# Optimization experiments

Measured on AMD Instinct MI355X. Metric: run time of the kernel, lower is better.

The kernel has to match this reference:

```python
import jax, jax.numpy as jnp
import numpy as np
from jax.scipy.linalg import solve_triangular

N, K, D = 131072, 8, 32  # samples, clusters, dims


def setup_inputs() -> dict:
    key = jax.random.key(0)
    k1, k2, k3, k4 = jax.random.split(key, 4)
    return {
        "X": jax.random.normal(k1, (N, D), dtype=jnp.float32),
        "mu": jax.random.normal(k2, (K, D), dtype=jnp.float32),
        "L": jax.random.normal(k3, (K, D, D), dtype=jnp.float32),
        "weights": jax.random.normal(k4, (K,), dtype=jnp.float32),
        "it": 0,
    }


def _mixture_log_likelihoods(X, mu, L, weights):
    K_, D_ = mu.shape
    LOG2PI = float(np.log(2.0 * np.pi))
    # update_covariances: A_k = L_k L_k^T + I  (always SPD -> cholesky succeeds)
    A = jnp.einsum('kab,kcb->kac', L, L) + jnp.eye(D_, dtype=L.dtype)
    Lc = jnp.linalg.cholesky(A)            # [K,D,D] lower Cholesky factors
    invLc = jnp.linalg.inv(Lc)             # [K,D,D]
    # all cluster pairs (cartesian_prod order: i outer, j inner)
    ii, jj = [g.reshape(-1) for g in jnp.meshgrid(jnp.arange(K_), jnp.arange(K_), indexing='ij')]
    Si, Sj = Lc[ii], Lc[jj]                # NOTE: original uses the CHOLESKY FACTORS here
    invSi, invSj = invLc[ii], invLc[jj]
    mui, muj = mu[ii], mu[jj]
    # _gaussian_product: sigma = inv(inv(Si)+inv(Sj)); mu = sigma @ (inv(Si) mu_i + inv(Sj) mu_j)
    sigma = jnp.linalg.inv(invSi + invSj)                      # [P,D,D]
    rhs = jnp.einsum('pab,pb->pa', invSi, mui) + jnp.einsum('pab,pb->pa', invSj, muj)
    mu_p = jnp.einsum('pab,pb->pa', sigma, rhs)                # [P,D]
    # _product_z: log(1/sqrt(det(2*pi*(Si+Sj))) * exp(-0.5 dmu^T inv(Si+Sj) dmu))
    S = Si + Sj
    dmu = mui - muj
    quad = -0.5 * jnp.einsum('pa,pab,pb->p', dmu, jnp.linalg.inv(S), dmu)
    z = -0.5 * jnp.log(jnp.linalg.det(2.0 * np.pi * S)) + quad  # [P]
    # _unormalised_pdf: lower-triangular solve against sigma (only lower triangle used)
    diff = X[None, :, :] - mu_p[:, None, :]                    # [P,N,D]
    m = solve_triangular(sigma, jnp.swapaxes(diff, 1, 2), lower=True)  # [P,D,N]
    ll = -0.5 * (jnp.sum(m * m, axis=1) + D_ * LOG2PI
                 + jnp.log(jnp.linalg.det(sigma))[:, None])    # [P,N]
    logw = jax.nn.log_softmax(weights)                         # softmax weights, then log
    logprob = z[:, None] + ll + logw[ii][:, None] + logw[jj][:, None]  # [P,N]
    return jnp.log(jnp.sum(jnp.exp(logprob), axis=0))          # [N]


def reference(X, mu, L, weights, it):
    ll = _mixture_log_likelihoods(X, mu, L, weights)
    return jax.scipy.special.logsumexp(ll, axis=0)  # scalar
```

## Files before the change

### kernel.cpp

```cpp
#include <hip/hip_runtime.h>

#define D 32
#define K 8
#define NPAIR 36
#define PROWS 576

#define PMOFF 0
#define WOFF 4608
#define C2OFF 4864
#define CMAXOFF 4900
#define LCOFF 4928
#define PARTOFF 13120

typedef float v2f __attribute__((ext_vector_type(2)));

__host__ __device__ constexpr int gidx(int i, int j) {
    return i * 8 + j - i * (i + 1) / 2;
}
__host__ __device__ constexpr int proff(int r) {
    return 4 * (r / 4 + 1) * (2 * (r / 4) + (r % 4));
}

__global__ __launch_bounds__(64) void setup1_kernel(
    const float* __restrict__ mu, const float* __restrict__ L,
    float* __restrict__ ws)
{
    __shared__ float sA[D][D + 1];
    __shared__ float sLc[D][D + 1];
    __shared__ float sI[D][D + 1];
    const int k = blockIdx.x;
    const int tid = threadIdx.x;
    const int i = tid & 31;

    for (int e = tid; e < D * D; e += 64) sI[e >> 5][e & 31] = L[k * D * D + e];
    __syncthreads();

    for (int e = tid; e < D * D; e += 64) {
        const int a = e >> 5, c = e & 31;
        float s = (a == c) ? 1.0f : 0.0f;
        #pragma unroll
        for (int b = 0; b < D; ++b) s = fmaf(sI[a][b], sI[c][b], s);
        sA[a][c] = s;
    }
    __syncthreads();

    float lrow[D];
    #pragma unroll
    for (int j = 0; j < D; ++j) {
        if (i == j) {
            float s = sA[j][j];
            #pragma unroll
            for (int b = 0; b < j; ++b) s = fmaf(-lrow[b], lrow[b], s);
            const float d = sqrtf(s);
            lrow[j] = d;
            #pragma unroll
            for (int b = 0; b < j; ++b) sLc[j][b] = lrow[b];
            sLc[j][j] = d;
        }
        __syncthreads();
        if (i > j) {
            float s = sA[i][j];
            #pragma unroll
            for (int b = 0; b < j; ++b) s = fmaf(-lrow[b], sLc[j][b], s);
            lrow[j] = s / sLc[j][j];
        }
    }
    __syncthreads();

    for (int e = tid; e < D * D; e += 64) {
        const int r = e >> 5, c = e & 31;
        ws[LCOFF + k * D * D + e] = (c <= r) ? sLc[r][c] : 0.0f;
    }

    {
        const int j = i;
        #pragma unroll
        for (int ii = 0; ii < D; ++ii) {
            float s = (ii == j) ? 1.0f : 0.0f;
            #pragma unroll
            for (int b = 0; b < ii; ++b) s = fmaf(-sLc[ii][b], sI[b][j], s);
            const float cii = s / sLc[ii][ii];
            sI[ii][j] = cii;
            const int w4 = 4 * (ii / 4 + 1);
            if (j < w4) ws[PMOFF + k * PROWS + proff(ii) + j] = cii;
        }
    }
    __syncthreads();

    {
        float s = 0.0f;
        #pragma unroll
        for (int b = 0; b < D; ++b) s = fmaf(sI[i][b], mu[k * D + b], s);
        ws[WOFF + k * D + i] = s;
    }
}

#define SLC(kk, r, c) sLc2[(kk) * 1024 + (r) * 32 + (c)]

__global__ __launch_bounds__(256) void setup2_kernel(
    const float* __restrict__ mu, const float* __restrict__ weights,
    float* __restrict__ ws)
{
    __shared__ float sLc2[K * D * D];
    __shared__ float sMu[K * D];
    __shared__ float sWt[K];
    __shared__ float sLogw[K];
    __shared__ float sCp[NPAIR];
    __shared__ float sCmax;
    const int tid = threadIdx.x;

    {
        const float4* src = (const float4*)(ws + LCOFF);
        float4* dst = (float4*)sLc2;
        #pragma unroll
        for (int e = 0; e < 8; ++e) dst[tid + 256 * e] = src[tid + 256 * e];
        sMu[tid] = mu[tid];
        if (tid < K) sWt[tid] = weights[tid];
    }
    __syncthreads();

    if (tid == 0) {
        float m = -INFINITY;
        for (int t = 0; t < K; ++t) m = fmaxf(m, sWt[t]);
        float s = 0.0f;
        for (int t = 0; t < K; ++t) s += expf(sWt[t] - m);
        const float lse = m + logf(s);
        for (int t = 0; t < K; ++t) sLogw[t] = sWt[t] - lse;
    }
    __syncthreads();

    if (tid < NPAIR) {
        int tt = tid, pi = 0;
        while (tt >= (K - pi)) { tt -= (K - pi); ++pi; }
        const int pj = pi + tt;
        const float LOG2PI = 1.8378770664093453f;
        float sumlogS = 0.0f, logdetsig = 0.0f;
        #pragma unroll
        for (int r = 0; r < D; ++r) {
            const float di = SLC(pi, r, r), dj = SLC(pj, r, r);
            sumlogS += logf(di + dj);
            logdetsig -= logf(1.0f / di + 1.0f / dj);
        }
        float v[D];
        float quad_acc = 0.0f;
        #pragma unroll
        for (int r = 0; r < D; ++r) {
            const float d0 = sMu[pi * D + r] - sMu[pj * D + r];
            float s = d0;
            #pragma unroll
            for (int b = 0; b < r; ++b)
                s = fmaf(-(SLC(pi, r, b) + SLC(pj, r, b)), v[b], s);
            v[r] = s / (SLC(pi, r, r) + SLC(pj, r, r));
            quad_acc = fmaf(d0, v[r], quad_acc);
        }
        const float quad = -0.5f * quad_acc;
        float c = quad - 0.5f * sumlogS - (float)D * LOG2PI - 0.5f * logdetsig
                  + sLogw[pi] + sLogw[pj];
        if (pi < pj) c += 0.6931471805599453f;
        sCp[tid] = c;
    }
    __syncthreads();
    if (tid == 0) {
        float m = -INFINITY;
        for (int t = 0; t < NPAIR; ++t) m = fmaxf(m, sCp[t]);
        sCmax = m;
        ws[CMAXOFF] = m;
    }
    __syncthreads();
    if (tid < NPAIR)
        ws[C2OFF + tid] = (sCp[tid] - sCmax) * 1.4426950408889634f;
}

#define XCHG 4864

__global__ __launch_bounds__(128, 2) void main_kernel(
    const float* __restrict__ X, const float* __restrict__ cst,
    float* __restrict__ partials, int nsamp)
{
    __shared__ __align__(16) float sBig[XCHG];
    __shared__ __align__(16) float sW[K * D];
    __shared__ float sC2[NPAIR];
    const int tid = threadIdx.x;
    const int wv = tid >> 6;
    const int lane = tid & 63;

    const int n0 = blockIdx.x * 128 + lane;
    const int n1 = n0 + 64;
    const int m0 = (n0 < nsamp) ? n0 : 0;
    const int m1 = (n1 < nsamp) ? n1 : 0;

    v2f xa[16], xb[16];
    {
        const float4* Xv0 = (const float4*)(X + m0 * D);
        const float4* Xv1 = (const float4*)(X + m1 * D);
        #pragma unroll
        for (int q = 0; q < 8; ++q) {
            const float4 t0 = Xv0[q];
            xa[2 * q]     = (v2f){t0.x, t0.y};
            xa[2 * q + 1] = (v2f){t0.z, t0.w};
            const float4 t1 = Xv1[q];
            xb[2 * q]     = (v2f){t1.x, t1.y};
            xb[2 * q + 1] = (v2f){t1.z, t1.w};
        }
    }

    {
        const float4* src = (const float4*)cst;
        float4* dst = (float4*)sBig;
        for (int e = tid; e < K * PROWS / 4; e += 128) dst[e] = src[e];
        const float4* srcw = (const float4*)(cst + WOFF);
        float4* dstw = (float4*)sW;
        if (tid < K * D / 4) dstw[tid] = srcw[tid];
        if (tid < NPAIR) sC2[tid] = cst[C2OFF + tid];
    }
    __syncthreads();

    v2f G2[NPAIR];
    #pragma unroll
    for (int t = 0; t < NPAIR; ++t) G2[t] = (v2f){0.0f, 0.0f};

    #pragma unroll
    for (int rh = 0; rh < 8; ++rh) {
        if ((rh & 1) == wv) {
            #pragma unroll
            for (int rr = 0; rr < 4; ++rr) {
                const int r = 4 * rh + rr;
                v2f ya[K], yb[K];
                #pragma unroll
                for (int k = 0; k < K; ++k) {
                    const float wvv = sW[k * D + r];
                    v2f a0 = (v2f){-wvv, 0.0f};
                    v2f a1 = (v2f){-wvv, 0.0f};
                    const float* Mr = sBig + k * PROWS + proff(r);
                    #pragma unroll
                    for (int c4 = 0; c4 <= rh; ++c4) {
                        const float4 m4 = *(const float4*)(Mr + 4 * c4);
                        const v2f mlo = (v2f){m4.x, m4.y};
                        const v2f mhi = (v2f){m4.z, m4.w};
                        a0 = __builtin_elementwise_fma(mlo, xa[2 * c4],     a0);
                        a1 = __builtin_elementwise_fma(mlo, xb[2 * c4],     a1);
                        a0 = __builtin_elementwise_fma(mhi, xa[2 * c4 + 1], a0);
                        a1 = __builtin_elementwise_fma(mhi, xb[2 * c4 + 1], a1);
                    }
                    ya[k] = a0;  yb[k] = a1;
                }
                v2f y2[K];
                #pragma unroll
                for (int k = 0; k < K; ++k)
                    y2[k] = (v2f){ya[k].x + ya[k].y, yb[k].x + yb[k].y};
                #pragma unroll
                for (int pi = 0; pi < K; ++pi)
                    #pragma unroll
                    for (int pj = pi; pj < K; ++pj)
                        G2[gidx(pi, pj)] = __builtin_elementwise_fma(
                            y2[pi], y2[pj], G2[gidx(pi, pj)]);
            }
        }
    }

    __syncthreads();

    if (wv == 1) {
        float2* xch = (float2*)sBig;
        #pragma unroll
        for (int t = 0; t < NPAIR; ++t)
            xch[t * 65 + lane] = make_float2(G2[t].x, G2[t].y);
    }
    __syncthreads();

    if (wv == 0) {
        const float2* xch = (const float2*)sBig;
        #pragma unroll
        for (int t = 0; t < NPAIR; ++t) {
            const float2 g = xch[t * 65 + lane];
            G2[t] += (v2f){g.x, g.y};
        }

        v2f acc2 = (v2f){0.0f, 0.0f};
        const float NH = -0.72134752044448170f;
        #pragma unroll
        for (int pi = 0; pi < K; ++pi)
            #pragma unroll
            for (int pj = pi; pj < K; ++pj) {
                const v2f q2 = __builtin_elementwise_fma(
                    (v2f){2.0f, 2.0f}, G2[gidx(pi, pj)],
                    G2[gidx(pi, pi)] + G2[gidx(pj, pj)]);
                const float c = sC2[gidx(pi, pj)];
                const v2f e2 = __builtin_elementwise_fma((v2f){NH, NH}, q2,
                                                         (v2f){c, c});
                acc2.x += exp2f(e2.x);
                acc2.y += exp2f(e2.y);
            }
        float acc = ((n0 < nsamp) ? acc2.x : 0.0f)
                  + ((n1 < nsamp) ? acc2.y : 0.0f);

        #pragma unroll
        for (int s = 1; s < 64; s <<= 1) acc += __shfl_xor(acc, s, 64);
        if (lane == 0) partials[blockIdx.x] = acc;
    }
}

__global__ __launch_bounds__(256) void finish_kernel(
    const float* __restrict__ partials, const float* __restrict__ ws,
    float* __restrict__ out, int nblk)
{
    __shared__ float sRed[4];
    const int tid = threadIdx.x;
    float acc = 0.0f;
    for (int e = tid; e < nblk; e += 256) acc += partials[e];
    #pragma unroll
    for (int s = 1; s < 64; s <<= 1) acc += __shfl_xor(acc, s, 64);
    if ((tid & 63) == 0) sRed[tid >> 6] = acc;
    __syncthreads();
    if (tid == 0) out[0] = ws[CMAXOFF] + logf(sRed[0] + sRed[1] + sRed[2] + sRed[3]);
}

extern "C" void kernel_launch(void* const* d_in, const int* in_sizes, int n_in,
                              void* d_out, int out_size, void* d_ws, size_t ws_size,
                              hipStream_t stream) {
    const float* X = (const float*)d_in[0];
    const float* mu = (const float*)d_in[1];
    const float* L = (const float*)d_in[2];
    const float* w = (const float*)d_in[3];
    float* wsf = (float*)d_ws;
    float* out = (float*)d_out;

    const int nsamp = in_sizes[0] / D;
    const int nblk = (nsamp + 127) / 128;

    setup1_kernel<<<K, 64, 0, stream>>>(mu, L, wsf);
    setup2_kernel<<<1, 256, 0, stream>>>(mu, w, wsf);
    main_kernel<<<nblk, 128, 0, stream>>>(X, wsf, wsf + PARTOFF, nsamp);
    finish_kernel<<<1, 256, 0, stream>>>(wsf + PARTOFF, wsf, out, nblk);
}
```

Baseline: 139.5 us.

## Merge setup kernels into one block and fold final reduction via ticket atomic

Combines the two setup kernels into a single 512-thread block that computes all eight Cholesky factors in shared memory. The pair constants are then computed directly from those factors, which removes the workspace round-trip of the factors. The W vectors are now obtained by forward substitution with shuffles instead of multiplying by the inverse. The separate finish kernel is removed: the last main-kernel block to arrive, detected with an atomic ticket, reduces the partials and writes the output. This cuts two kernel launches, at the cost of serializing the eight factorizations onto one CU and adding an atomic and fences to every main block.

Result: slower. 161.8 us (+16.0%).

```diff
diff --git a/kernel.cpp b/kernel.cpp
--- a/kernel.cpp
+++ b/kernel.cpp
@@ -9,7 +9,7 @@
 #define WOFF 4608
 #define C2OFF 4864
 #define CMAXOFF 4900
-#define LCOFF 4928
+#define TICKOFF 4904
 #define PARTOFF 13120
 
 typedef float v2f __attribute__((ext_vector_type(2)));
@@ -21,26 +21,40 @@
     return 4 * (r / 4 + 1) * (2 * (r / 4) + (r % 4));
 }
 
-__global__ __launch_bounds__(64) void setup1_kernel(
+__global__ __launch_bounds__(512) void setup_kernel(
     const float* __restrict__ mu, const float* __restrict__ L,
-    float* __restrict__ ws)
+    const float* __restrict__ weights, float* __restrict__ ws)
 {
-    __shared__ float sA[D][D + 1];
-    __shared__ float sLc[D][D + 1];
-    __shared__ float sI[D][D + 1];
-    const int k = blockIdx.x;
+    __shared__ float sA[K][D][D + 1];
+    __shared__ float sMu[K * D];
+    __shared__ float sLogw[K];
+    __shared__ float sCp[NPAIR];
+    __shared__ float sCmax;
+
     const int tid = threadIdx.x;
-    const int i = tid & 31;
-
-    for (int e = tid; e < D * D; e += 64) sI[e >> 5][e & 31] = L[k * D * D + e];
-    __syncthreads();
-
-    for (int e = tid; e < D * D; e += 64) {
+    const int k = tid >> 6;
+    const int t64 = tid & 63;
+    const int i = t64 & 31;
+
+    if (tid < K * D) sMu[tid] = mu[tid];
+    for (int e = t64; e < D * D; e += 64) sA[k][e >> 5][e & 31] = L[k * D * D + e];
+    __syncthreads();
+
+    float areg[16];
+    #pragma unroll
+    for (int q = 0; q < 16; ++q) {
+        const int e = t64 + 64 * q;
         const int a = e >> 5, c = e & 31;
         float s = (a == c) ? 1.0f : 0.0f;
         #pragma unroll
-        for (int b = 0; b < D; ++b) s = fmaf(sI[a][b], sI[c][b], s);
-        sA[a][c] = s;
+        for (int b = 0; b < D; ++b) s = fmaf(sA[k][a][b], sA[k][c][b], s);
+        areg[q] = s;
+    }
+    __syncthreads();
+    #pragma unroll
+    for (int q = 0; q < 16; ++q) {
+        const int e = t64 + 64 * q;
+        sA[k][e >> 5][e & 31] = areg[q];
     }
     __syncthreads();
 
@@ -48,84 +62,65 @@
     #pragma unroll
     for (int j = 0; j < D; ++j) {
         if (i == j) {
-            float s = sA[j][j];
+            float s = sA[k][j][j];
             #pragma unroll
             for (int b = 0; b < j; ++b) s = fmaf(-lrow[b], lrow[b], s);
             const float d = sqrtf(s);
             lrow[j] = d;
             #pragma unroll
-            for (int b = 0; b < j; ++b) sLc[j][b] = lrow[b];
-            sLc[j][j] = d;
+            for (int b = 0; b < j; ++b) sA[k][j][b] = lrow[b];
+            sA[k][j][j] = d;
         }
         __syncthreads();
         if (i > j) {
-            float s = sA[i][j];
-            #pragma unroll
-            for (int b = 0; b < j; ++b) s = fmaf(-lrow[b], sLc[j][b], s);
-            lrow[j] = s / sLc[j][j];
-        }
-    }
-    __syncthreads();
-
-    for (int e = tid; e < D * D; e += 64) {
-        const int r = e >> 5, c = e & 31;
-        ws[LCOFF + k * D * D + e] = (c <= r) ? sLc[r][c] : 0.0f;
-    }
+            float s = sA[k][i][j];
+            #pragma unroll
+            for (int b = 0; b < j; ++b) s = fmaf(-lrow[b], sA[k][j][b], s);
+            lrow[j] = s / sA[k][j][j];
+        }
+    }
+    __syncthreads();
 
     {
         const int j = i;
+        float col[D];
         #pragma unroll
         for (int ii = 0; ii < D; ++ii) {
             float s = (ii == j) ? 1.0f : 0.0f;
             #pragma unroll
-            for (int b = 0; b < ii; ++b) s = fmaf(-sLc[ii][b], sI[b][j], s);
-            const float cii = s / sLc[ii][ii];
-            sI[ii][j] = cii;
+            for (int b = 0; b < ii; ++b) s = fmaf(-sA[k][ii][b], col[b], s);
+            const float cii = s / sA[k][ii][ii];
+            col[ii] = cii;
             const int w4 = 4 * (ii / 4 + 1);
             if (j < w4) ws[PMOFF + k * PROWS + proff(ii) + j] = cii;
         }
     }
-    __syncthreads();
 
     {
+        float s = sMu[k * D + i];
+        #pragma unroll
+        for (int j2 = 0; j2 < D; ++j2) {
+            const float wj = __shfl(s, j2, 32) / sA[k][j2][j2];
+            if (i == j2) ws[WOFF + k * D + i] = wj;
+            if (i > j2) s = fmaf(-sA[k][i][j2], wj, s);
+        }
+    }
+    __syncthreads();
+
+    if (tid == 0) {
+        float wl[K];
+        #pragma unroll
+        for (int t = 0; t < K; ++t) wl[t] = weights[t];
+        float m = -INFINITY;
+        #pragma unroll
+        for (int t = 0; t < K; ++t) m = fmaxf(m, wl[t]);
         float s = 0.0f;
         #pragma unroll
-        for (int b = 0; b < D; ++b) s = fmaf(sI[i][b], mu[k * D + b], s);
-        ws[WOFF + k * D + i] = s;
-    }
-}
-
-#define SLC(kk, r, c) sLc2[(kk) * 1024 + (r) * 32 + (c)]
-
-__global__ __launch_bounds__(256) void setup2_kernel(
-    const float* __restrict__ mu, const float* __restrict__ weights,
-    float* __restrict__ ws)
-{
-    __shared__ float sLc2[K * D * D];
-    __shared__ float sMu[K * D];
-    __shared__ float sWt[K];
-    __shared__ float sLogw[K];
-    __shared__ float sCp[NPAIR];
-    __shared__ float sCmax;
-    const int tid = threadIdx.x;
-
-    {
-        const float4* src = (const float4*)(ws + LCOFF);
-        float4* dst = (float4*)sLc2;
-        #pragma unroll
-        for (int e = 0; e < 8; ++e) dst[tid + 256 * e] = src[tid + 256 * e];
-        sMu[tid] = mu[tid];
-        if (tid < K) sWt[tid] = weights[tid];
-    }
-    __syncthreads();
-
-    if (tid == 0) {
-        float m = -INFINITY;
-        for (int t = 0; t < K; ++t) m = fmaxf(m, sWt[t]);
-        float s = 0.0f;
-        for (int t = 0; t < K; ++t) s += expf(sWt[t] - m);
+        for (int t = 0; t < K; ++t) s += expf(wl[t] - m);
         const float lse = m + logf(s);
-        for (int t = 0; t < K; ++t) sLogw[t] = sWt[t] - lse;
+        #pragma unroll
+        for (int t = 0; t < K; ++t) sLogw[t] = wl[t] - lse;
+        *(unsigned int*)(ws + TICKOFF) = 0u;
     }
     __syncthreads();
 
@@ -137,7 +132,7 @@
         float sumlogS = 0.0f, logdetsig = 0.0f;
         #pragma unroll
         for (int r = 0; r < D; ++r) {
-            const float di = SLC(pi, r, r), dj = SLC(pj, r, r);
+            const float di = sA[pi][r][r], dj = sA[pj][r][r];
             sumlogS += logf(di + dj);
             logdetsig -= logf(1.0f / di + 1.0f / dj);
         }
@@ -149,8 +144,8 @@
             float s = d0;
             #pragma unroll
             for (int b = 0; b < r; ++b)
-                s = fmaf(-(SLC(pi, r, b) + SLC(pj, r, b)), v[b], s);
-            v[r] = s / (SLC(pi, r, r) + SLC(pj, r, r));
+                s = fmaf(-(sA[pi][r][b] + sA[pj][r][b]), v[b], s);
+            v[r] = s / (sA[pi][r][r] + sA[pj][r][r]);
             quad_acc = fmaf(d0, v[r], quad_acc);
         }
         const float quad = -0.5f * quad_acc;
@@ -175,11 +170,14 @@
 
 __global__ __launch_bounds__(128, 2) void main_kernel(
     const float* __restrict__ X, const float* __restrict__ cst,
-    float* __restrict__ partials, int nsamp)
+    float* __restrict__ partials, float* __restrict__ out,
+    unsigned int* __restrict__ ticket, int nsamp, int nblk)
 {
     __shared__ __align__(16) float sBig[XCHG];
     __shared__ __align__(16) float sW[K * D];
     __shared__ float sC2[NPAIR];
+    __shared__ int sIsLast;
+    __shared__ float sRed[2];
     const int tid = threadIdx.x;
     const int wv = tid >> 6;
     const int lane = tid & 63;
@@ -296,23 +294,25 @@
 
         #pragma unroll
         for (int s = 1; s < 64; s <<= 1) acc += __shfl_xor(acc, s, 64);
-        if (lane == 0) partials[blockIdx.x] = acc;
-    }
-}
-
-__global__ __launch_bounds__(256) void finish_kernel(
-    const float* __restrict__ partials, const float* __restrict__ ws,
-    float* __restrict__ out, int nblk)
-{
-    __shared__ float sRed[4];
-    const int tid = threadIdx.x;
-    float acc = 0.0f;
-    for (int e = tid; e < nblk; e += 256) acc += partials[e];
-    #pragma unroll
-    for (int s = 1; s < 64; s <<= 1) acc += __shfl_xor(acc, s, 64);
-    if ((tid & 63) == 0) sRed[tid >> 6] = acc;
-    __syncthreads();
-    if (tid == 0) out[0] = ws[CMAXOFF] + logf(sRed[0] + sRed[1] + sRed[2] + sRed[3]);
+        if (lane == 0) {
+            partials[blockIdx.x] = acc;
+            __threadfence();
+            const unsigned prev = atomicAdd(ticket, 1u);
+            sIsLast = (prev == (unsigned)(nblk - 1)) ? 1 : 0;
+        }
+    }
+    __syncthreads();
+
+    if (sIsLast) {
+        __threadfence();
+        float a2 = 0.0f;
+        for (int e = tid; e < nblk; e += 128) a2 += partials[e];
+        #pragma unroll
+        for (int s = 1; s < 64; s <<= 1) a2 += __shfl_xor(a2, s, 64);
+        if (lane == 0) sRed[wv] = a2;
+        __syncthreads();
+        if (tid == 0) out[0] = cst[CMAXOFF] + logf(sRed[0] + sRed[1]);
+    }
 }
 
 extern "C" void kernel_launch(void* const* d_in, const int* in_sizes, int n_in,
@@ -328,8 +328,8 @@
     const int nsamp = in_sizes[0] / D;
     const int nblk = (nsamp + 127) / 128;
 
-    setup1_kernel<<<K, 64, 0, stream>>>(mu, L, wsf);
-    setup2_kernel<<<1, 256, 0, stream>>>(mu, w, wsf);
-    main_kernel<<<nblk, 128, 0, stream>>>(X, wsf, wsf + PARTOFF, nsamp);
-    finish_kernel<<<1, 256, 0, stream>>>(wsf + PARTOFF, wsf, out, nblk);
-}
+    setup_kernel<<<1, 512, 0, stream>>>(mu, L, w, wsf);
+    main_kernel<<<nblk, 128, 0, stream>>>(X, wsf, wsf + PARTOFF, out,
+                                          (unsigned int*)(wsf + TICKOFF),
+                                          nsamp, nblk);
+}
```

## Split row-blocks across four waves and fuse final reduction via ticket

Applied to the files above, without the earlier changes.

The main kernel now runs with 256 threads, so four waves share the same 128 samples. Each wave takes a pair of row-blocks (rh and 7-rh), which evens out the triangular work. The per-wave partial Gram sums are combined through shared memory in three chunks. The separate finish kernel is removed: a global atomic ticket lets the last block do the final sum and log, saving one launch. The cost is more LDS exchange traffic and extra barriers, with unchanged per-thread register pressure under a higher occupancy bound.

Measured after the change: 360.7 us. 2.59x slower.

```diff
diff --git a/kernel.cpp b/kernel.cpp
--- a/kernel.cpp
+++ b/kernel.cpp
@@ -9,6 +9,7 @@
 #define WOFF 4608
 #define C2OFF 4864
 #define CMAXOFF 4900
+#define TICKOFF 4904
 #define LCOFF 4928
 #define PARTOFF 13120
 
@@ -126,6 +127,7 @@
         for (int t = 0; t < K; ++t) s += expf(sWt[t] - m);
         const float lse = m + logf(s);
         for (int t = 0; t < K; ++t) sLogw[t] = sWt[t] - lse;
+        *(unsigned int*)(ws + TICKOFF) = 0u;
     }
     __syncthreads();
 
@@ -171,15 +173,16 @@
         ws[C2OFF + tid] = (sCp[tid] - sCmax) * 1.4426950408889634f;
 }
 
-#define XCHG 4864
-
-__global__ __launch_bounds__(128, 2) void main_kernel(
+__global__ __launch_bounds__(256, 4) void main_kernel(
     const float* __restrict__ X, const float* __restrict__ cst,
-    float* __restrict__ partials, int nsamp)
+    float* __restrict__ partials, float* __restrict__ out,
+    unsigned int* __restrict__ ticket, int nsamp, int nblk)
 {
-    __shared__ __align__(16) float sBig[XCHG];
+    __shared__ __align__(16) float sBig[4864];
     __shared__ __align__(16) float sW[K * D];
     __shared__ float sC2[NPAIR];
+    __shared__ int sIsLast;
+    __shared__ float sRed[4];
     const int tid = threadIdx.x;
     const int wv = tid >> 6;
     const int lane = tid & 63;
@@ -207,7 +210,7 @@
     {
         const float4* src = (const float4*)cst;
         float4* dst = (float4*)sBig;
-        for (int e = tid; e < K * PROWS / 4; e += 128) dst[e] = src[e];
+        for (int e = tid; e < K * PROWS / 4; e += 256) dst[e] = src[e];
         const float4* srcw = (const float4*)(cst + WOFF);
         float4* dstw = (float4*)sW;
         if (tid < K * D / 4) dstw[tid] = srcw[tid];
@@ -221,7 +224,7 @@
 
     #pragma unroll
     for (int rh = 0; rh < 8; ++rh) {
-        if ((rh & 1) == wv) {
+        if (((rh < 4) ? rh : 7 - rh) == wv) {
             #pragma unroll
             for (int rr = 0; rr < 4; ++rr) {
                 const int r = 4 * rh + rr;
@@ -260,22 +263,32 @@
 
     __syncthreads();
 
-    if (wv == 1) {
+    {
         float2* xch = (float2*)sBig;
         #pragma unroll
-        for (int t = 0; t < NPAIR; ++t)
-            xch[t * 65 + lane] = make_float2(G2[t].x, G2[t].y);
-    }
-    __syncthreads();
+        for (int chunk = 0; chunk < 3; ++chunk) {
+            if (wv > 0) {
+                #pragma unroll
+                for (int t = 0; t < 12; ++t)
+                    xch[((wv - 1) * 12 + t) * 64 + lane] =
+                        make_float2(G2[chunk * 12 + t].x, G2[chunk * 12 + t].y);
+            }
+            __syncthreads();
+            if (wv == 0) {
+                #pragma unroll
+                for (int t = 0; t < 12; ++t) {
+                    const float2 g0 = xch[(0 * 12 + t) * 64 + lane];
+                    const float2 g1 = xch[(1 * 12 + t) * 64 + lane];
+                    const float2 g2 = xch[(2 * 12 + t) * 64 + lane];
+                    G2[chunk * 12 + t] +=
+                        (v2f){g0.x + g1.x + g2.x, g0.y + g1.y + g2.y};
+                }
+            }
+            __syncthreads();
+        }
+    }
 
     if (wv == 0) {
-        const float2* xch = (const float2*)sBig;
-        #pragma unroll
-        for (int t = 0; t < NPAIR; ++t) {
-            const float2 g = xch[t * 65 + lane];
-            G2[t] += (v2f){g.x, g.y};
-        }
-
         v2f acc2 = (v2f){0.0f, 0.0f};
         const float NH = -0.72134752044448170f;
         #pragma unroll
@@ -296,23 +309,27 @@
 
         #pragma unroll
         for (int s = 1; s < 64; s <<= 1) acc += __shfl_xor(acc, s, 64);
-        if (lane == 0) partials[blockIdx.x] = acc;
-    }
-}
-
-__global__ __launch_bounds__(256) void finish_kernel(
-    const float* __restrict__ partials, const float* __restrict__ ws,
-    float* __restrict__ out, int nblk)
-{
-    __shared__ float sRed[4];
-    const int tid = threadIdx.x;
-    float acc = 0.0f;
-    for (int e = tid; e < nblk; e += 256) acc += partials[e];
-    #pragma unroll
-    for (int s = 1; s < 64; s <<= 1) acc += __shfl_xor(acc, s, 64);
-    if ((tid & 63) == 0) sRed[tid >> 6] = acc;
-    __syncthreads();
-    if (tid == 0) out[0] = ws[CMAXOFF] + logf(sRed[0] + sRed[1] + sRed[2] + sRed[3]);
+        if (lane == 0) {
+            partials[blockIdx.x] = acc;
+            __threadfence();
+            const unsigned prev = atomicAdd(ticket, 1u);
+            sIsLast = (prev == (unsigned)(nblk - 1)) ? 1 : 0;
+        }
+    }
+    __syncthreads();
+
+    if (sIsLast) {
+        __threadfence();
+        float a2 = 0.0f;
+        for (int e = tid; e < nblk; e += 256) a2 += partials[e];
+        #pragma unroll
+        for (int s = 1; s < 64; s <<= 1) a2 += __shfl_xor(a2, s, 64);
+        if (lane == 0) sRed[wv] = a2;
+        __syncthreads();
+        if (tid == 0)
+            out[0] = cst[CMAXOFF]
+                   + logf(sRed[0] + sRed[1] + sRed[2] + sRed[3]);
+    }
 }
 
 extern "C" void kernel_launch(void* const* d_in, const int* in_sizes, int n_in,
@@ -330,6 +347,7 @@
 
     setup1_kernel<<<K, 64, 0, stream>>>(mu, L, wsf);
     setup2_kernel<<<1, 256, 0, stream>>>(mu, w, wsf);
-    main_kernel<<<nblk, 128, 0, stream>>>(X, wsf, wsf + PARTOFF, nsamp);
-    finish_kernel<<<1, 256, 0, stream>>>(wsf + PARTOFF, wsf, out, nblk);
-}
+    main_kernel<<<nblk, 256, 0, stream>>>(X, wsf, wsf + PARTOFF, out,
+                                          (unsigned int*)(wsf + TICKOFF),
+                                          nsamp, nblk);
+}
```
